# Optimization experiments

Hardware: AMD Instinct MI355X
Metric: run time of the kernel (lower is better)

Reference implementation:

```python
import jax, jax.numpy as jnp
import numpy as np

NUM_HEADS = 12
HEAD_DIM = 64
HIDDEN = NUM_HEADS * HEAD_DIM
AGENT_NUM = 40
MAX_POS = 2048
SCALE = HEAD_DIM ** -0.5


def _split_heads(x):
    # [b, s, hidden] -> [b, h, s, d]
    b, s, _ = x.shape
    return x.reshape(b, s, NUM_HEADS, HEAD_DIM).transpose(0, 2, 1, 3)


def _agent_pool(q, agent_num):
    # F.interpolate(q[None], size=(agent_num, dim), mode='bilinear', align_corners=False)
    # width (dim) is unchanged so it reduces to 1D linear interp along seq axis.
    b, s, dim = q.shape
    src = (jnp.arange(agent_num, dtype=q.dtype) + 0.5) * (s / agent_num) - 0.5
    src = jnp.clip(src, 0.0, s - 1.0)
    lo = jnp.floor(src).astype(jnp.int32)
    hi = jnp.minimum(lo + 1, s - 1)
    w = (src - lo.astype(q.dtype))[None, :, None]  # [1, A, 1]
    return q[:, lo, :] * (1.0 - w) + q[:, hi, :] * w  # [b, A, dim]


def setup_inputs() -> dict:
    key = jax.random.key(0)
    ks = jax.random.split(key, 6)
    bs, S = 16, 2048
    return {
        "hidden_states": jax.random.normal(ks[0], (bs, S, HIDDEN), jnp.float32),
        "attention_mask": jnp.zeros((bs, 1, 1, S), jnp.float32),
        "Wq": jax.random.normal(ks[1], (HIDDEN, HIDDEN), jnp.float32) * 0.02,
        "bq": jnp.zeros((HIDDEN,), jnp.float32),
        "Wk": jax.random.normal(ks[2], (HIDDEN, HIDDEN), jnp.float32) * 0.02,
        "bk": jnp.zeros((HIDDEN,), jnp.float32),
        "Wv": jax.random.normal(ks[3], (HIDDEN, HIDDEN), jnp.float32) * 0.02,
        "bv": jnp.zeros((HIDDEN,), jnp.float32),
        "dist_emb": jax.random.normal(ks[4], (2 * MAX_POS - 1, HEAD_DIM), jnp.float32) * 0.02,
    }


def reference(hidden_states, attention_mask, Wq, bq, Wk, bk, Wv, bv, dist_emb):
    bs, S, dim = hidden_states.shape
    q = hidden_states @ Wq + bq          # [b, S, hidden] (== query_layer flattened back)
    k = hidden_states @ Wk + bk
    v = hidden_states @ Wv + bv
    q_layer = _split_heads(q)            # [b, h, S, d]
    k_layer = _split_heads(k)
    v_layer = _split_heads(v)

    agent = _agent_pool(q, AGENT_NUM)    # [b, A, hidden]
    agent_layer = _split_heads(agent)    # [b, h, A, d]

    # stage 1: agent -> KV, with relative-key position bias
    d1 = jnp.arange(AGENT_NUM)[:, None] - jnp.arange(S)[None, :] + (MAX_POS - 1)
    pe1 = dist_emb[d1]                   # [A, S, d]
    bias1 = jnp.einsum('bhad,asd->bhas', agent_layer, pe1)
    score1 = jnp.einsum('bhad,bhsd->bhas', agent_layer * SCALE, k_layer) + bias1
    score1 = score1 + attention_mask     # [b,1,1,S] broadcasts over (h, A)
    p1 = jax.nn.softmax(score1, axis=-1)
    agent_v = jnp.einsum('bhas,bhsd->bhad', p1, v_layer)  # [b, h, A, d]

    # stage 2: query -> agents, with relative-key position bias
    d2 = jnp.arange(S)[:, None] - jnp.arange(AGENT_NUM)[None, :] + (MAX_POS - 1)
    pe2 = dist_emb[d2]                   # [S, A, d]
    bias2 = jnp.einsum('bhsd,sad->bhsa', q_layer, pe2)
    score2 = jnp.einsum('bhsd,bhad->bhsa', q_layer * SCALE, agent_layer) + bias2
    q_mask = jnp.swapaxes(attention_mask, -1, -2)  # [b,1,S,1]
    score2 = score2 + q_mask
    p2 = jax.nn.softmax(score2, axis=-1)
    x = jnp.einsum('bhsa,bhad->bhsd', p2, agent_v)  # [b, h, S, d]
    return x.transpose(0, 2, 1, 3).reshape(bs, S, dim)
```

## Files before the change

### kernel.cpp

```cpp
#include <hip/hip_runtime.h>
#include <math.h>

#define B_ 16
#define S_ 2048
#define H_ 12
#define D_ 64
#define HID 768
#define A_ 40
#define SCALE_ 0.125f
#define CH1 8
#define SUBT 64
#define NSUB 4

typedef __attribute__((ext_vector_type(8))) short short8v;
typedef __attribute__((ext_vector_type(4))) float f32x4;
typedef __attribute__((ext_vector_type(16))) float f32x16;

__device__ __forceinline__ unsigned f2bf_bits(float x) {
    unsigned u = __float_as_uint(x);
    return (u + 0x7FFFu + ((u >> 16) & 1u)) >> 16;
}

__device__ __forceinline__ void split1(float v, unsigned short& h, unsigned short& l) {
    __bf16 bh = (__bf16)v;
    float hf = (float)bh;
    __bf16 bl = (__bf16)(v - hf);
    h = __builtin_bit_cast(unsigned short, bh);
    l = __builtin_bit_cast(unsigned short, bl);
}

__device__ __forceinline__ void split8c(const float* x, int4& hi, int4& lo) {
    unsigned h[8], l[8];
#pragma unroll
    for (int i = 0; i < 8; i++) {
        __bf16 bh = (__bf16)x[i];
        float hf = (float)bh;
        __bf16 bl = (__bf16)(x[i] - hf);
        h[i] = (unsigned)__builtin_bit_cast(unsigned short, bh);
        l[i] = (unsigned)__builtin_bit_cast(unsigned short, bl);
    }
    hi = make_int4((int)(h[0] | (h[1] << 16)), (int)(h[2] | (h[3] << 16)),
                   (int)(h[4] | (h[5] << 16)), (int)(h[6] | (h[7] << 16)));
    lo = make_int4((int)(l[0] | (l[1] << 16)), (int)(l[2] | (l[3] << 16)),
                   (int)(l[4] | (l[5] << 16)), (int)(l[6] | (l[7] << 16)));
}

__global__ void wt_convert(const float* __restrict__ Wq, const float* __restrict__ Wk,
                           const float* __restrict__ Wv,
                           unsigned short* __restrict__ Wth, unsigned short* __restrict__ Wtl)
{
    int idx = blockIdx.x * 256 + threadIdx.x;
    if (idx >= 3 * 192 * 768) return;
    int n  = idx % 768;
    int kc = (idx / 768) % 192;
    int z  = idx / (768 * 192);
    const float* W = (z == 0) ? Wq : (z == 1) ? Wk : Wv;
    unsigned short h4[4], l4[4];
#pragma unroll
    for (int i = 0; i < 4; i++) {
        float x = W[(size_t)(4 * kc + i) * HID + n];
        unsigned hb = f2bf_bits(x);
        float hf = __uint_as_float(hb << 16);
        h4[i] = (unsigned short)hb;
        l4[i] = (unsigned short)f2bf_bits(x - hf);
    }
    size_t o = ((size_t)z * HID + n) * HID + 4 * kc;
    *(ushort4*)&Wth[o] = make_ushort4(h4[0], h4[1], h4[2], h4[3]);
    *(ushort4*)&Wtl[o] = make_ushort4(l4[0], l4[1], l4[2], l4[3]);
}

__global__ void dist_frag(const float* __restrict__ dist,
                          unsigned short* __restrict__ DFh, unsigned short* __restrict__ DFl)
{
    int g = blockIdx.x * 256 + threadIdx.x;
    if (g >= 256 * 2 * 64) return;
    int lane = g & 63;
    int ks = (g >> 6) & 1;
    int u  = g >> 7;
    int row = 8 + u * 16 + (lane & 15);
    int col = ks * 32 + ((lane >> 4) << 3);
    float xv[8];
#pragma unroll
    for (int j = 0; j < 8; j++)
        xv[j] = (row < 4095) ? dist[(size_t)row * D_ + col + j] : 0.f;
    int4 hi, lo;
    split8c(xv, hi, lo);
    *(int4*)&DFh[(size_t)g * 8] = hi;
    *(int4*)&DFl[(size_t)g * 8] = lo;
}

__global__ void dist_frag0(const float* __restrict__ dist,
                           unsigned short* __restrict__ Dh, unsigned short* __restrict__ Dl)
{
    int g = blockIdx.x * 256 + threadIdx.x;
    if (g >= 131 * 2 * 64) return;
    int lane = g & 63;
    int ks = (g >> 6) & 1;
    int u  = g >> 7;
    int row = u * 16 + (lane & 15);
    int col = ks * 32 + ((lane >> 4) << 3);
    float xv[8];
#pragma unroll
    for (int j = 0; j < 8; j++) xv[j] = dist[(size_t)row * D_ + col + j];
    int4 hi, lo;
    split8c(xv, hi, lo);
    *(int4*)&Dh[(size_t)g * 8] = hi;
    *(int4*)&Dl[(size_t)g * 8] = lo;
}

__global__ void ag_frag(const float* __restrict__ Ag,
                        unsigned short* __restrict__ Gh, unsigned short* __restrict__ Gl,
                        float scale)
{
    int g = blockIdx.x * 256 + threadIdx.x;
    if (g >= 192 * 3 * 2 * 64) return;
    int lane = g & 63;
    int r = g >> 6;
    int ks = r & 1; r >>= 1;
    int at = r % 3;
    int bh = r / 3;
    int a = at * 16 + (lane & 15);
    int col = ks * 32 + ((lane >> 4) << 3);
    float xv[8];
#pragma unroll
    for (int j = 0; j < 8; j++)
        xv[j] = (a < A_) ? scale * Ag[((size_t)bh * A_ + a) * D_ + col + j] : 0.f;
    int4 hi, lo;
    split8c(xv, hi, lo);
    *(int4*)&Gh[(size_t)g * 8] = hi;
    *(int4*)&Gl[(size_t)g * 8] = lo;
}

__global__ void avt_frag(const float* __restrict__ AgV,
                         unsigned short* __restrict__ Vh, unsigned short* __restrict__ Vl)
{
    int g = blockIdx.x * 256 + threadIdx.x;
    if (g >= 192 * 4 * 2 * 64) return;
    int lane = g & 63;
    int r = g >> 6;
    int ks = r & 1; r >>= 1;
    int nt = r & 3;
    int bh = r >> 2;
    int d = nt * 16 + (lane & 15);
    int a0 = ks * 32 + ((lane >> 4) << 3);
    float xv[8];
#pragma unroll
    for (int j = 0; j < 8; j++) {
        int a = a0 + j;
        xv[j] = (a < A_) ? AgV[((size_t)bh * A_ + a) * D_ + d] : 0.f;
    }
    int4 hi, lo;
    split8c(xv, hi, lo);
    *(int4*)&Vh[(size_t)g * 8] = hi;
    *(int4*)&Vl[(size_t)g * 8] = lo;
}

__global__ __launch_bounds__(512, 2) void qkv_z(
    const float* __restrict__ X,
    const unsigned short* __restrict__ Wth, const unsigned short* __restrict__ Wtl,
    const float* __restrict__ bq, const float* __restrict__ bk, const float* __restrict__ bv,
    float* __restrict__ Q, float* __restrict__ K, float* __restrict__ V)
{
    const int L   = blockIdx.x;
    const int k8  = L & 7, sl_ = L >> 3;
    const int mt  = k8 * 32 + sl_ / 9;
    const int sub = sl_ % 9;
    const int nt  = sub % 3, zz = sub / 3;
    const int m0 = mt * 128, n0 = nt * 256;

    const float* __restrict__ bias = (zz == 0) ? bq : (zz == 1) ? bk : bv;
    float* __restrict__ Out        = (zz == 0) ? Q  : (zz == 1) ? K  : V;
    const unsigned short* __restrict__ Bhg = Wth + (size_t)zz * HID * HID;
    const unsigned short* __restrict__ Blg = Wtl + (size_t)zz * HID * HID;

    __shared__ unsigned short Ah[128][40];
    __shared__ unsigned short Al[128][40];
    __shared__ unsigned short Bh[256][40];
    __shared__ unsigned short Bl[256][40];

    const int t = threadIdx.x;
    const int lane = t & 63, w = t >> 6;
    const int wm = (w & 1) * 64, wn = (w >> 1) * 64;
    const int r32 = lane & 31, kh = lane >> 5;

    const int sr = t >> 2, sca = (t & 3) * 8;
    const int sb = t >> 1, scb = (t & 1) * 16;

    f32x16 acc[2][2];
#pragma unroll
    for (int i = 0; i < 2; i++)
#pragma unroll
        for (int j = 0; j < 2; j++)
#pragma unroll
            for (int p = 0; p < 16; p++) acc[i][j][p] = 0.f;

    for (int k0 = 0; k0 < HID; k0 += 32) {
        float xv[8];
        const float* xp = X + (size_t)(m0 + sr) * HID + k0 + sca;
        float4 f0 = *(const float4*)xp;
        float4 f1 = *(const float4*)(xp + 4);
        xv[0] = f0.x; xv[1] = f0.y; xv[2] = f0.z; xv[3] = f0.w;
        xv[4] = f1.x; xv[5] = f1.y; xv[6] = f1.z; xv[7] = f1.w;
        int4 ah, al;
        split8c(xv, ah, al);
        size_t bo = (size_t)(n0 + sb) * HID + k0 + scb;
        int4 bh0 = *(const int4*)&Bhg[bo];
        int4 bh1 = *(const int4*)&Bhg[bo + 8];
        int4 bl0 = *(const int4*)&Blg[bo];
        int4 bl1 = *(const int4*)&Blg[bo + 8];

        __syncthreads();
        *(int4*)&Ah[sr][sca] = ah;
        *(int4*)&Al[sr][sca] = al;
        *(int4*)&Bh[sb][scb]     = bh0;  *(int4*)&Bh[sb][scb + 8] = bh1;
        *(int4*)&Bl[sb][scb]     = bl0;  *(int4*)&Bl[sb][scb + 8] = bl1;
        __syncthreads();

#pragma unroll
        for (int ks = 0; ks < 2; ks++) {
            const int ko = ks * 16 + kh * 8;
            short8v a_h[2], a_l[2], b_h[2], b_l[2];
#pragma unroll
            for (int i = 0; i < 2; i++) {
                a_h[i] = *(const short8v*)&Ah[wm + i * 32 + r32][ko];
                a_l[i] = *(const short8v*)&Al[wm + i * 32 + r32][ko];
                b_h[i] = *(const short8v*)&Bh[wn + i * 32 + r32][ko];
                b_l[i] = *(const short8v*)&Bl[wn + i * 32 + r32][ko];
            }
#pragma unroll
            for (int i = 0; i < 2; i++)
#pragma unroll
                for (int j = 0; j < 2; j++) {
                    acc[i][j] = __builtin_amdgcn_mfma_f32_32x32x16_bf16(a_h[i], b_h[j], acc[i][j], 0, 0, 0);
                    acc[i][j] = __builtin_amdgcn_mfma_f32_32x32x16_bf16(a_l[i], b_h[j], acc[i][j], 0, 0, 0);
                    acc[i][j] = __builtin_amdgcn_mfma_f32_32x32x16_bf16(a_h[i], b_l[j], acc[i][j], 0, 0, 0);
                }
        }
    }

    const float scl = (zz == 1) ? SCALE_ : 1.0f;
#pragma unroll
    for (int j = 0; j < 2; j++) {
        int n = n0 + wn + j * 32 + r32;
        float bj = bias[n];
        int h = n >> 6, d = n & 63;
#pragma unroll
        for (int i = 0; i < 2; i++) {
#pragma unroll
            for (int p = 0; p < 16; p++) {
                int m = m0 + wm + i * 32 + (p & 3) + 8 * (p >> 2) + 4 * kh;
                int b = m >> 11, s = m & 2047;
                Out[(((size_t)b * H_ + h) * S_ + s) * D_ + d] = (acc[i][j][p] + bj) * scl;
            }
        }
    }
}

__global__ void agent_pool(const float* __restrict__ Q, float* __restrict__ Ag)
{
    int idx = blockIdx.x * 256 + threadIdx.x;
    if (idx >= B_ * H_ * A_ * D_) return;
    int d  = idx & 63;
    int a  = (idx >> 6) % A_;
    int bh = idx / (A_ * D_);
    float src = ((float)a + 0.5f) * (2048.0f / 40.0f) - 0.5f;
    src = fminf(fmaxf(src, 0.0f), 2047.0f);
    int lo = (int)floorf(src);
    int hi = min(lo + 1, S_ - 1);
    float w = src - (float)lo;
    const float* base = Q + (size_t)bh * (S_ * D_);
    Ag[idx] = base[lo * D_ + d] * (1.0f - w) + base[hi * D_ + d] * w;
}

__global__ __launch_bounds__(256, 2) void stage1_mfma(
    const float* __restrict__ Kl, const float* __restrict__ Vl,
    const unsigned short* __restrict__ AG1h, const unsigned short* __restrict__ AG1l,
    const unsigned short* __restrict__ D0h,  const unsigned short* __restrict__ D0l,
    const float* __restrict__ mask,
    float* __restrict__ Pacc, float* __restrict__ Pm, float* __restrict__ Pl)
{
    const int q  = blockIdx.x;
    const int bh = blockIdx.y;
    const int b  = bh / H_;
    const int s0 = q * (NSUB * SUBT);
    const float* __restrict__ kb = Kl + (size_t)bh * (S_ * D_);
    const float* __restrict__ vb = Vl + (size_t)bh * (S_ * D_);

    __shared__ unsigned short KFh[4096], KFl[4096];
    __shared__ unsigned short VTh[4096], VTl[4096];
    __shared__ float sc[SUBT][52];
    __shared__ float scp[112][52];
    __shared__ float pm6[6][A_];
    __shared__ float mrow[A_], lrow[A_], resc[A_], mrw[SUBT];

    const int t = threadIdx.x;
    const int lane = t & 63, w = t >> 6;
    const int fr = lane & 15, kg = lane >> 4;

    if (t < A_) { mrow[t] = -INFINITY; lrow[t] = 0.0f; }

    f32x4 acc3[3];
#pragma unroll
    for (int at = 0; at < 3; at++) acc3[at] = (f32x4){0.f, 0.f, 0.f, 0.f};

    for (int st = 0; st < NSUB; st++) {
        const int sb = s0 + st * SUBT;
        const int u0 = (1984 - sb) >> 4;

        __syncthreads();

        {
            const int r = t >> 2, c0 = (t & 3) * 16;
            const float* kp = kb + (size_t)(sb + r) * D_ + c0;
            float xa[8], xb[8];
            float4 f0 = *(const float4*)(kp);
            float4 f1 = *(const float4*)(kp + 4);
            float4 f2 = *(const float4*)(kp + 8);
            float4 f3 = *(const float4*)(kp + 12);
            xa[0]=f0.x; xa[1]=f0.y; xa[2]=f0.z; xa[3]=f0.w;
            xa[4]=f1.x; xa[5]=f1.y; xa[6]=f1.z; xa[7]=f1.w;
            xb[0]=f2.x; xb[1]=f2.y; xb[2]=f2.z; xb[3]=f2.w;
            xb[4]=f3.x; xb[5]=f3.y; xb[6]=f3.z; xb[7]=f3.w;
            int4 h0, l0, h1, l1;
            split8c(xa, h0, l0);
            split8c(xb, h1, l1);
            const int tsr = r >> 4, frr = r & 15;
            const int c8a = (t & 3) * 2, c8b = c8a + 1;
            const int oa = ((tsr * 2 + (c8a >> 2)) * 64 + (((c8a & 3) << 4) | frr)) * 8;
            const int ob = ((tsr * 2 + (c8b >> 2)) * 64 + (((c8b & 3) << 4) | frr)) * 8;
            *(int4*)&KFh[oa] = h0;  *(int4*)&KFl[oa] = l0;
            *(int4*)&KFh[ob] = h1;  *(int4*)&KFl[ob] = l1;
        }
        {
            const int r = t >> 2, c0 = (t & 3) * 16;
            const float* vp = vb + (size_t)(sb + r) * D_ + c0;
            float vv[16];
            float4 g0 = *(const float4*)(vp);
            float4 g1 = *(const float4*)(vp + 4);
            float4 g2 = *(const float4*)(vp + 8);
            float4 g3 = *(const float4*)(vp + 12);
            vv[0]=g0.x; vv[1]=g0.y; vv[2]=g0.z; vv[3]=g0.w;
            vv[4]=g1.x; vv[5]=g1.y; vv[6]=g1.z; vv[7]=g1.w;
            vv[8]=g2.x; vv[9]=g2.y; vv[10]=g2.z; vv[11]=g2.w;
            vv[12]=g3.x; vv[13]=g3.y; vv[14]=g3.z; vv[15]=g3.w;
            const int ks2 = r >> 5, kgp = (r & 31) >> 3, e = r & 7;
#pragma unroll
            for (int jj = 0; jj < 16; jj++) {
                int d = c0 + jj;
                int off = (((d >> 4) * 2 + ks2) * 64 + kgp * 16 + (d & 15)) * 8 + e;
                unsigned short h, l;
                split1(vv[jj], h, l);
                VTh[off] = h; VTl[off] = l;
            }
        }
        if (t < SUBT) mrw[t] = mask[(size_t)b * S_ + sb + t];
        __syncthreads();

        {
            const int ts = w;
#pragma unroll
            for (int at = 0; at < 3; at++) {
                f32x4 a4 = (f32x4){0.f, 0.f, 0.f, 0.f};
#pragma unroll
                for (int ks = 0; ks < 2; ks++) {
                    size_t oA = ((((size_t)bh * 3 + at) * 2 + ks) * 64 + lane) * 8;
                    short8v gh = *(const short8v*)&AG1h[oA];
                    short8v gl = *(const short8v*)&AG1l[oA];
                    short8v kh2 = *(const short8v*)&KFh[((ts * 2 + ks) * 64 + lane) * 8];
                    short8v kl2 = *(const short8v*)&KFl[((ts * 2 + ks) * 64 + lane) * 8];
                    a4 = __builtin_amdgcn_mfma_f32_16x16x32_bf16(gh, kh2, a4, 0, 0, 0);
                    a4 = __builtin_amdgcn_mfma_f32_16x16x32_bf16(gl, kh2, a4, 0, 0, 0);
                    a4 = __builtin_amdgcn_mfma_f32_16x16x32_bf16(gh, kl2, a4, 0, 0, 0);
                }
                *(f32x4*)&sc[ts * 16 + fr][at * 16 + kg * 4] = a4;
            }
        }
        for (int ut = w; ut < 7; ut += 4) {
            const int u = u0 + ut;
#pragma unroll
            for (int at = 0; at < 3; at++) {
                f32x4 a4 = (f32x4){0.f, 0.f, 0.f, 0.f};
#pragma unroll
                for (int ks = 0; ks < 2; ks++) {
                    size_t oA = ((((size_t)bh * 3 + at) * 2 + ks) * 64 + lane) * 8;
                    short8v gh = *(const short8v*)&AG1h[oA];
                    short8v gl = *(const short8v*)&AG1l[oA];
                    size_t oD = (((size_t)u * 2 + ks) * 64 + lane) * 8;
                    short8v dh = *(const short8v*)&D0h[oD];
                    short8v dl = *(const short8v*)&D0l[oD];
                    a4 = __builtin_amdgcn_mfma_f32_16x16x32_bf16(gh, dh, a4, 0, 0, 0);
                    a4 = __builtin_amdgcn_mfma_f32_16x16x32_bf16(gl, dh, a4, 0, 0, 0);
                    a4 = __builtin_amdgcn_mfma_f32_16x16x32_bf16(gh, dl, a4, 0, 0, 0);
                }
                *(f32x4*)&scp[ut * 16 + fr][at * 16 + kg * 4] = a4;
            }
        }
        __syncthreads();

        for (int i = t; i < SUBT * A_; i += 256) {
            int rr = i / 40, aa = i - rr * 40;
            sc[rr][aa] += scp[aa + 63 - rr][aa] + mrw[rr];
        }
        __syncthreads();
        if (t < 240) {
            int a = t % 40, r6 = t / 40;
            float mx = -INFINITY;
            for (int i = r6; i < SUBT; i += 6) mx = fmaxf(mx, sc[i][a]);
            pm6[r6][a] = mx;
        }
        __syncthreads();
        if (t < A_) {
            float lm = pm6[0][t];
#pragma unroll
            for (int r6 = 1; r6 < 6; r6++) lm = fmaxf(lm, pm6[r6][t]);
            float mnew = fmaxf(mrow[t], lm);
            resc[t] = __expf(mrow[t] - mnew);
            mrow[t] = mnew;
        }
        __syncthreads();
        for (int i = t; i < SUBT * A_; i += 256) {
            int rr = i / 40, aa = i - rr * 40;
            sc[rr][aa] = __expf(sc[rr][aa] - mrow[aa]);
        }
        __syncthreads();
        if (t < 240) {
            int a = t % 40, r6 = t / 40;
            float sm = 0.0f;
            for (int i = r6; i < SUBT; i += 6) sm += sc[i][a];
            pm6[r6][a] = sm;
        }
        __syncthreads();
        if (t < A_) {
            float ls = pm6[0][t] + pm6[1][t] + pm6[2][t] + pm6[3][t] + pm6[4][t] + pm6[5][t];
            lrow[t] = lrow[t] * resc[t] + ls;
        }
        __syncthreads();

        for (int g = t; g < 384; g += 256) {
            int pl = g & 63;
            int c = g >> 6;
            int at = c >> 1, ks2 = c & 1;
            int a = at * 16 + (pl & 15);
            int sl0 = ks2 * 32 + (pl >> 4) * 8;
            float xv[8];
#pragma unroll
            for (int e = 0; e < 8; e++)
                xv[e] = (a < A_) ? sc[sl0 + e][a] : 0.f;
            int4 hi, lo;
            split8c(xv, hi, lo);
            *(int4*)&KFh[g * 8] = hi;
            *(int4*)&KFl[g * 8] = lo;
        }
        __syncthreads();

        {
            const int dt = w;
#pragma unroll
            for (int at = 0; at < 3; at++) {
                f32x4 a4 = acc3[at];
#pragma unroll
                for (int p = 0; p < 4; p++) {
                    int a = at * 16 + kg * 4 + p;
                    float rs = (a < A_) ? resc[a] : 0.f;
                    a4[p] *= rs;
                }
#pragma unroll
                for (int ks2 = 0; ks2 < 2; ks2++) {
                    short8v ph = *(const short8v*)&KFh[((at * 2 + ks2) * 64 + lane) * 8];
                    short8v pll = *(const short8v*)&KFl[((at * 2 + ks2) * 64 + lane) * 8];
                    short8v vh = *(const short8v*)&VTh[((dt * 2 + ks2) * 64 + lane) * 8];
                    short8v vl = *(const short8v*)&VTl[((dt * 2 + ks2) * 64 + lane) * 8];
                    a4 = __builtin_amdgcn_mfma_f32_16x16x32_bf16(ph, vh, a4, 0, 0, 0);
                    a4 = __builtin_amdgcn_mfma_f32_16x16x32_bf16(pll, vh, a4, 0, 0, 0);
                    a4 = __builtin_amdgcn_mfma_f32_16x16x32_bf16(ph, vl, a4, 0, 0, 0);
                }
                acc3[at] = a4;
            }
        }
    }
    __syncthreads();

    {
        const int dt = w;
#pragma unroll
        for (int at = 0; at < 3; at++) {
#pragma unroll
            for (int p = 0; p < 4; p++) {
                int a = at * 16 + kg * 4 + p;
                if (a < A_)
                    Pacc[(((size_t)(bh * CH1 + q) * A_) + a) * D_ + dt * 16 + fr] = acc3[at][p];
            }
        }
    }
    if (t < A_) {
        Pm[(size_t)(bh * CH1 + q) * A_ + t] = mrow[t];
        Pl[(size_t)(bh * CH1 + q) * A_ + t] = lrow[t];
    }
}

__global__ __launch_bounds__(256) void stage1_reduce(
    const float* __restrict__ Pacc, const float* __restrict__ Pm,
    const float* __restrict__ Pl, float* __restrict__ AgV)
{
    const int bh = blockIdx.x;
    const int t = threadIdx.x;
    __shared__ float F[CH1][A_], Linv[A_];
    if (t < A_) {
        float M = -INFINITY;
#pragma unroll
        for (int q = 0; q < CH1; q++) M = fmaxf(M, Pm[(size_t)(bh * CH1 + q) * A_ + t]);
        float L = 0.0f;
#pragma unroll
        for (int q = 0; q < CH1; q++) {
            float f = __expf(Pm[(size_t)(bh * CH1 + q) * A_ + t] - M);
            F[q][t] = f;
            L = fmaf(f, Pl[(size_t)(bh * CH1 + q) * A_ + t], L);
        }
        Linv[t] = 1.0f / L;
    }
    __syncthreads();
#pragma unroll
    for (int ii = 0; ii < 3; ii++) {
        int i = t + ii * 256;
        if (i < A_ * 16) {
            int a = i >> 4, d4 = i & 15;
            float4 s4 = make_float4(0.f, 0.f, 0.f, 0.f);
            for (int q = 0; q < CH1; q++) {
                float f = F[q][a];
                float4 p4 = *(const float4*)&Pacc[(((size_t)(bh * CH1 + q) * A_) + a) * D_ + d4 * 4];
                s4.x = fmaf(f, p4.x, s4.x);
                s4.y = fmaf(f, p4.y, s4.y);
                s4.z = fmaf(f, p4.z, s4.z);
                s4.w = fmaf(f, p4.w, s4.w);
            }
            float inv = Linv[a];
            s4.x *= inv; s4.y *= inv; s4.z *= inv; s4.w *= inv;
            *(float4*)&AgV[(size_t)bh * (A_ * D_) + a * D_ + d4 * 4] = s4;
        }
    }
}

__global__ __launch_bounds__(256, 2) void stage2_mfma(
    const float* __restrict__ Qg,
    const unsigned short* __restrict__ AGFh, const unsigned short* __restrict__ AGFl,
    const unsigned short* __restrict__ DFh,  const unsigned short* __restrict__ DFl,
    const unsigned short* __restrict__ AVFh, const unsigned short* __restrict__ AVFl,
    float* __restrict__ Out)
{
    const int sb8 = blockIdx.x;
    const int bh  = blockIdx.y;
    const int b = bh / H_, h = bh % H_;

    __shared__ unsigned short Qfh[8 * 64 * 8], Qfl[8 * 64 * 8];
    __shared__ float scm[64][52];
    __shared__ float scp[64][68];
    __shared__ unsigned short PAh[64][72], PAl[64][72];

    const int t = threadIdx.x;
    const int lane = t & 63, ts = t >> 6;
    const int fr = lane & 15, kg = lane >> 4;

    short8v agh[3][2], agl[3][2];
#pragma unroll
    for (int at = 0; at < 3; at++)
#pragma unroll
        for (int ks = 0; ks < 2; ks++) {
            size_t o = ((((size_t)bh * 3 + at) * 2 + ks) * 64 + lane) * 8;
            agh[at][ks] = *(const short8v*)&AGFh[o];
            agl[at][ks] = *(const short8v*)&AGFl[o];
        }

    const int r = t >> 2, c0 = (t & 3) * 16;
    const int tsr = r >> 4, frr = r & 15;
    const int c8a = (t & 3) * 2, c8b = c8a + 1;
    const int oa = ((tsr * 2 + (c8a >> 2)) * 64 + (((c8a & 3) << 4) | frr)) * 8;
    const int ob = ((tsr * 2 + (c8b >> 2)) * 64 + (((c8b & 3) << 4) | frr)) * 8;
    const float* qbase = Qg + ((size_t)bh * S_ + sb8 * 256 + r) * D_ + c0;

    {
        float4 f0 = *(const float4*)(qbase);
        float4 f1 = *(const float4*)(qbase + 4);
        float4 f2 = *(const float4*)(qbase + 8);
        float4 f3 = *(const float4*)(qbase + 12);
        float xa[8] = {f0.x, f0.y, f0.z, f0.w, f1.x, f1.y, f1.z, f1.w};
        float xb[8] = {f2.x, f2.y, f2.z, f2.w, f3.x, f3.y, f3.z, f3.w};
        int4 h0, l0, h1, l1;
        split8c(xa, h0, l0);
        split8c(xb, h1, l1);
        *(int4*)&Qfh[oa] = h0;  *(int4*)&Qfl[oa] = l0;
        *(int4*)&Qfh[ob] = h1;  *(int4*)&Qfl[ob] = l1;
    }
    __syncthreads();

    for (int c = 0; c < 4; c++) {
        const int s0 = sb8 * 256 + c * 64;
        const int base_u = (s0 >> 4) + 125;

        short8v qh[2], ql[2];
#pragma unroll
        for (int ks = 0; ks < 2; ks++) {
            qh[ks] = *(const short8v*)&Qfh[((ts * 2 + ks) * 64 + lane) * 8];
            ql[ks] = *(const short8v*)&Qfl[((ts * 2 + ks) * 64 + lane) * 8];
        }
        float4 nf0, nf1, nf2, nf3;
        if (c < 3) {
            const float* np = qbase + (size_t)(c + 1) * 64 * D_;
            nf0 = *(const float4*)(np);
            nf1 = *(const float4*)(np + 4);
            nf2 = *(const float4*)(np + 8);
            nf3 = *(const float4*)(np + 12);
        }

#pragma unroll
        for (int at = 0; at < 3; at++) {
            f32x4 acc = (f32x4){0.f, 0.f, 0.f, 0.f};
#pragma unroll
            for (int ks = 0; ks < 2; ks++) {
                acc = __builtin_amdgcn_mfma_f32_16x16x32_bf16(agh[at][ks], qh[ks], acc, 0, 0, 0);
                acc = __builtin_amdgcn_mfma_f32_16x16x32_bf16(agl[at][ks], qh[ks], acc, 0, 0, 0);
                acc = __builtin_amdgcn_mfma_f32_16x16x32_bf16(agh[at][ks], ql[ks], acc, 0, 0, 0);
            }
            *(f32x4*)&scm[ts * 16 + fr][at * 16 + kg * 4] = acc;
        }
#pragma unroll
        for (int o4 = 0; o4 < 4; o4++) {
            f32x4 acc = (f32x4){0.f, 0.f, 0.f, 0.f};
            const int u = base_u + ts + o4;
#pragma unroll
            for (int ks = 0; ks < 2; ks++) {
                size_t o = (((size_t)u * 2 + ks) * 64 + lane) * 8;
                short8v chv = *(const short8v*)&DFh[o];
                short8v clv = *(const short8v*)&DFl[o];
                acc = __builtin_amdgcn_mfma_f32_16x16x32_bf16(chv, qh[ks], acc, 0, 0, 0);
                acc = __builtin_amdgcn_mfma_f32_16x16x32_bf16(clv, qh[ks], acc, 0, 0, 0);
                acc = __builtin_amdgcn_mfma_f32_16x16x32_bf16(chv, ql[ks], acc, 0, 0, 0);
            }
            *(f32x4*)&scp[ts * 16 + fr][o4 * 16 + kg * 4] = acc;
        }
        __syncthreads();

        if (c < 3) {
            float xa[8] = {nf0.x, nf0.y, nf0.z, nf0.w, nf1.x, nf1.y, nf1.z, nf1.w};
            float xb[8] = {nf2.x, nf2.y, nf2.z, nf2.w, nf3.x, nf3.y, nf3.z, nf3.w};
            int4 h0, l0, h1, l1;
            split8c(xa, h0, l0);
            split8c(xb, h1, l1);
            *(int4*)&Qfh[oa] = h0;  *(int4*)&Qfl[oa] = l0;
            *(int4*)&Qfh[ob] = h1;  *(int4*)&Qfl[ob] = l1;
        }
        {
            const int rr = t >> 2, dq = t & 3;
            const int base = (rr & 15) + 39;
            float val[10];
#pragma unroll
            for (int i = 0; i < 10; i++) {
                int a = dq * 10 + i;
                val[i] = scm[rr][a] + scp[rr][base - a];
            }
            float mx = -INFINITY;
#pragma unroll
            for (int i = 0; i < 10; i++) mx = fmaxf(mx, val[i]);
            mx = fmaxf(mx, __shfl_xor(mx, 1));
            mx = fmaxf(mx, __shfl_xor(mx, 2));
            float sum = 0.f;
#pragma unroll
            for (int i = 0; i < 10; i++) { val[i] = __expf(val[i] - mx); sum += val[i]; }
            sum += __shfl_xor(sum, 1);
            sum += __shfl_xor(sum, 2);
            float inv = 1.0f / sum;
            unsigned* ph = (unsigned*)&PAh[rr][0];
            unsigned* pl = (unsigned*)&PAl[rr][0];
#pragma unroll
            for (int i = 0; i < 5; i++) {
                unsigned short h0, l0, h1, l1;
                split1(val[2 * i] * inv, h0, l0);
                split1(val[2 * i + 1] * inv, h1, l1);
                ph[dq * 5 + i] = (unsigned)h0 | ((unsigned)h1 << 16);
                pl[dq * 5 + i] = (unsigned)l0 | ((unsigned)l1 << 16);
            }
#pragma unroll
            for (int i = 0; i < 3; i++) { ph[20 + dq * 3 + i] = 0u; pl[20 + dq * 3 + i] = 0u; }
        }
        __syncthreads();

        short8v ph8[2], pl8[2];
#pragma unroll
        for (int ks = 0; ks < 2; ks++) {
            ph8[ks] = *(const short8v*)&PAh[ts * 16 + fr][ks * 32 + kg * 8];
            pl8[ks] = *(const short8v*)&PAl[ts * 16 + fr][ks * 32 + kg * 8];
        }
#pragma unroll
        for (int nt = 0; nt < 4; nt++) {
            f32x4 acc = (f32x4){0.f, 0.f, 0.f, 0.f};
#pragma unroll
            for (int ks = 0; ks < 2; ks++) {
                size_t o = ((((size_t)bh * 4 + nt) * 2 + ks) * 64 + lane) * 8;
                short8v vh = *(const short8v*)&AVFh[o];
                short8v vl = *(const short8v*)&AVFl[o];
                acc = __builtin_amdgcn_mfma_f32_16x16x32_bf16(ph8[ks], vh, acc, 0, 0, 0);
                acc = __builtin_amdgcn_mfma_f32_16x16x32_bf16(pl8[ks], vh, acc, 0, 0, 0);
                acc = __builtin_amdgcn_mfma_f32_16x16x32_bf16(ph8[ks], vl, acc, 0, 0, 0);
            }
            const int d = nt * 16 + fr;
            float* op = Out + ((size_t)b * S_ + s0 + ts * 16 + kg * 4) * HID + h * D_ + d;
#pragma unroll
            for (int rr = 0; rr < 4; rr++)
                op[(size_t)rr * HID] = acc[rr];
        }
        __syncthreads();
    }
}

extern "C" void kernel_launch(void* const* d_in, const int* in_sizes, int n_in,
                              void* d_out, int out_size, void* d_ws, size_t ws_size,
                              hipStream_t stream) {
    const float* hs   = (const float*)d_in[0];
    const float* mask = (const float*)d_in[1];
    const float* Wq   = (const float*)d_in[2];
    const float* bq   = (const float*)d_in[3];
    const float* Wk   = (const float*)d_in[4];
    const float* bk   = (const float*)d_in[5];
    const float* Wv   = (const float*)d_in[6];
    const float* bv   = (const float*)d_in[7];
    const float* dist = (const float*)d_in[8];
    float* out = (float*)d_out;

    float* ws = (float*)d_ws;
    const size_t QKV = (size_t)B_ * H_ * S_ * D_;
    const size_t AG  = (size_t)B_ * H_ * A_ * D_;
    float* Q     = ws;
    float* K     = ws + QKV;
    float* V     = ws + 2 * QKV;
    float* Agent = ws + 3 * QKV;
    float* AgV   = Agent + AG;
    float* Pacc  = AgV + AG;
    float* Pm    = Pacc + (size_t)B_ * H_ * CH1 * A_ * D_;
    float* Pl    = Pm + (size_t)B_ * H_ * CH1 * A_;
    unsigned short* Wth = (unsigned short*)(Pl + (size_t)B_ * H_ * CH1 * A_);
    unsigned short* Wtl = Wth + (size_t)3 * HID * HID;
    unsigned short* DFh = Wtl + (size_t)3 * HID * HID;
    unsigned short* DFl = DFh + (size_t)262144;
    unsigned short* AGFh = DFl + (size_t)262144;
    unsigned short* AGFl = AGFh + (size_t)589824;
    unsigned short* AVFh = AGFl + (size_t)589824;
    unsigned short* AVFl = AVFh + (size_t)786432;
    unsigned short* AG1h = AVFl + (size_t)786432;
    unsigned short* AG1l = AG1h + (size_t)589824;
    unsigned short* D0h  = AG1l + (size_t)589824;
    unsigned short* D0l  = D0h + (size_t)134144;

    wt_convert<<<(3 * 192 * 768 + 255) / 256, 256, 0, stream>>>(Wq, Wk, Wv, Wth, Wtl);
    dist_frag<<<(256 * 2 * 64 + 255) / 256, 256, 0, stream>>>(dist, DFh, DFl);
    dist_frag0<<<(131 * 2 * 64 + 255) / 256, 256, 0, stream>>>(dist, D0h, D0l);
    qkv_z<<<2304, 512, 0, stream>>>(hs, Wth, Wtl, bq, bk, bv, Q, K, V);
    agent_pool<<<(B_ * H_ * A_ * D_ + 255) / 256, 256, 0, stream>>>(Q, Agent);
    ag_frag<<<(192 * 3 * 2 * 64 + 255) / 256, 256, 0, stream>>>(Agent, AGFh, AGFl, SCALE_);
    ag_frag<<<(192 * 3 * 2 * 64 + 255) / 256, 256, 0, stream>>>(Agent, AG1h, AG1l, 1.0f);
    dim3 g1(CH1, B_ * H_);
    stage1_mfma<<<g1, 256, 0, stream>>>(K, V, AG1h, AG1l, D0h, D0l, mask, Pacc, Pm, Pl);
    stage1_reduce<<<B_ * H_, 256, 0, stream>>>(Pacc, Pm, Pl, AgV);
    avt_frag<<<(192 * 4 * 2 * 64 + 255) / 256, 256, 0, stream>>>(AgV, AVFh, AVFl);
    dim3 g2(8, B_ * H_);
    stage2_mfma<<<g2, 256, 0, stream>>>(Q, AGFh, AGFl, DFh, DFl, AVFh, AVFl, out);
}
```

Before: 563.4 us.

## Merge preconversion kernels, fuse agent pool with fragments, register-load Q in stage2

Three weight and dist conversion kernels are merged into one launch, and agent pooling is fused with both agent fragment conversions in a per-(b,h) kernel using shared memory. Stage2 now loads Q directly into MFMA fragment registers per lane instead of staging through LDS, drops a trailing barrier, and raises the launch-bounds occupancy hint to 3. This cuts launch overhead, intermediate global traffic and LDS/sync cost, at the risk of register pressure from the higher occupancy target and a possible race on the reused shared buffers now that the end-of-loop barrier is gone.

Measured after the change: 582.8 us. 3.4% more time.

```diff
diff --git a/kernel.cpp b/kernel.cpp
--- a/kernel.cpp
+++ b/kernel.cpp
@@ -45,90 +45,68 @@
                    (int)(l[4] | (l[5] << 16)), (int)(l[6] | (l[7] << 16)));
 }
 
-__global__ void wt_convert(const float* __restrict__ Wq, const float* __restrict__ Wk,
-                           const float* __restrict__ Wv,
-                           unsigned short* __restrict__ Wth, unsigned short* __restrict__ Wtl)
+#define WT_BLKS 1728
+#define DF_BLKS 128
+#define D0_BLKS 66
+__global__ __launch_bounds__(256) void preconvert(
+    const float* __restrict__ Wq, const float* __restrict__ Wk, const float* __restrict__ Wv,
+    const float* __restrict__ dist,
+    unsigned short* __restrict__ Wth, unsigned short* __restrict__ Wtl,
+    unsigned short* __restrict__ DFh, unsigned short* __restrict__ DFl,
+    unsigned short* __restrict__ D0h, unsigned short* __restrict__ D0l)
 {
-    int idx = blockIdx.x * 256 + threadIdx.x;
-    if (idx >= 3 * 192 * 768) return;
-    int n  = idx % 768;
-    int kc = (idx / 768) % 192;
-    int z  = idx / (768 * 192);
-    const float* W = (z == 0) ? Wq : (z == 1) ? Wk : Wv;
-    unsigned short h4[4], l4[4];
-#pragma unroll
-    for (int i = 0; i < 4; i++) {
-        float x = W[(size_t)(4 * kc + i) * HID + n];
-        unsigned hb = f2bf_bits(x);
-        float hf = __uint_as_float(hb << 16);
-        h4[i] = (unsigned short)hb;
-        l4[i] = (unsigned short)f2bf_bits(x - hf);
-    }
-    size_t o = ((size_t)z * HID + n) * HID + 4 * kc;
-    *(ushort4*)&Wth[o] = make_ushort4(h4[0], h4[1], h4[2], h4[3]);
-    *(ushort4*)&Wtl[o] = make_ushort4(l4[0], l4[1], l4[2], l4[3]);
-}
-
-__global__ void dist_frag(const float* __restrict__ dist,
-                          unsigned short* __restrict__ DFh, unsigned short* __restrict__ DFl)
-{
-    int g = blockIdx.x * 256 + threadIdx.x;
-    if (g >= 256 * 2 * 64) return;
-    int lane = g & 63;
-    int ks = (g >> 6) & 1;
-    int u  = g >> 7;
-    int row = 8 + u * 16 + (lane & 15);
-    int col = ks * 32 + ((lane >> 4) << 3);
-    float xv[8];
-#pragma unroll
-    for (int j = 0; j < 8; j++)
-        xv[j] = (row < 4095) ? dist[(size_t)row * D_ + col + j] : 0.f;
-    int4 hi, lo;
-    split8c(xv, hi, lo);
-    *(int4*)&DFh[(size_t)g * 8] = hi;
-    *(int4*)&DFl[(size_t)g * 8] = lo;
-}
-
-__global__ void dist_frag0(const float* __restrict__ dist,
-                           unsigned short* __restrict__ Dh, unsigned short* __restrict__ Dl)
-{
-    int g = blockIdx.x * 256 + threadIdx.x;
-    if (g >= 131 * 2 * 64) return;
-    int lane = g & 63;
-    int ks = (g >> 6) & 1;
-    int u  = g >> 7;
-    int row = u * 16 + (lane & 15);
-    int col = ks * 32 + ((lane >> 4) << 3);
-    float xv[8];
-#pragma unroll
-    for (int j = 0; j < 8; j++) xv[j] = dist[(size_t)row * D_ + col + j];
-    int4 hi, lo;
-    split8c(xv, hi, lo);
-    *(int4*)&Dh[(size_t)g * 8] = hi;
-    *(int4*)&Dl[(size_t)g * 8] = lo;
-}
-
-__global__ void ag_frag(const float* __restrict__ Ag,
-                        unsigned short* __restrict__ Gh, unsigned short* __restrict__ Gl,
-                        float scale)
-{
-    int g = blockIdx.x * 256 + threadIdx.x;
-    if (g >= 192 * 3 * 2 * 64) return;
-    int lane = g & 63;
-    int r = g >> 6;
-    int ks = r & 1; r >>= 1;
-    int at = r % 3;
-    int bh = r / 3;
-    int a = at * 16 + (lane & 15);
-    int col = ks * 32 + ((lane >> 4) << 3);
-    float xv[8];
-#pragma unroll
-    for (int j = 0; j < 8; j++)
-        xv[j] = (a < A_) ? scale * Ag[((size_t)bh * A_ + a) * D_ + col + j] : 0.f;
-    int4 hi, lo;
-    split8c(xv, hi, lo);
-    *(int4*)&Gh[(size_t)g * 8] = hi;
-    *(int4*)&Gl[(size_t)g * 8] = lo;
+    const int bx = blockIdx.x;
+    const int t = threadIdx.x;
+    if (bx < WT_BLKS) {
+        int idx = bx * 256 + t;
+        if (idx >= 3 * 192 * 768) return;
+        int n  = idx % 768;
+        int kc = (idx / 768) % 192;
+        int z  = idx / (768 * 192);
+        const float* W = (z == 0) ? Wq : (z == 1) ? Wk : Wv;
+        unsigned short h4[4], l4[4];
+#pragma unroll
+        for (int i = 0; i < 4; i++) {
+            float x = W[(size_t)(4 * kc + i) * HID + n];
+            unsigned hb = f2bf_bits(x);
+            float hf = __uint_as_float(hb << 16);
+            h4[i] = (unsigned short)hb;
+            l4[i] = (unsigned short)f2bf_bits(x - hf);
+        }
+        size_t o = ((size_t)z * HID + n) * HID + 4 * kc;
+        *(ushort4*)&Wth[o] = make_ushort4(h4[0], h4[1], h4[2], h4[3]);
+        *(ushort4*)&Wtl[o] = make_ushort4(l4[0], l4[1], l4[2], l4[3]);
+    } else if (bx < WT_BLKS + DF_BLKS) {
+        int g = (bx - WT_BLKS) * 256 + t;
+        int lane = g & 63;
+        int ks = (g >> 6) & 1;
+        int u  = g >> 7;
+        int row = 8 + u * 16 + (lane & 15);
+        int col = ks * 32 + ((lane >> 4) << 3);
+        float xv[8];
+#pragma unroll
+        for (int j = 0; j < 8; j++)
+            xv[j] = (row < 4095) ? dist[(size_t)row * D_ + col + j] : 0.f;
+        int4 hi, lo;
+        split8c(xv, hi, lo);
+        *(int4*)&DFh[(size_t)g * 8] = hi;
+        *(int4*)&DFl[(size_t)g * 8] = lo;
+    } else {
+        int g = (bx - WT_BLKS - DF_BLKS) * 256 + t;
+        if (g >= 131 * 2 * 64) return;
+        int lane = g & 63;
+        int ks = (g >> 6) & 1;
+        int u  = g >> 7;
+        int row = u * 16 + (lane & 15);
+        int col = ks * 32 + ((lane >> 4) << 3);
+        float xv[8];
+#pragma unroll
+        for (int j = 0; j < 8; j++) xv[j] = dist[(size_t)row * D_ + col + j];
+        int4 hi, lo;
+        split8c(xv, hi, lo);
+        *(int4*)&D0h[(size_t)g * 8] = hi;
+        *(int4*)&D0l[(size_t)g * 8] = lo;
+    }
 }
 
 __global__ void avt_frag(const float* __restrict__ AgV,
@@ -256,20 +234,44 @@
     }
 }
 
-__global__ void agent_pool(const float* __restrict__ Q, float* __restrict__ Ag)
+__global__ __launch_bounds__(256) void agpool_frag(
+    const float* __restrict__ Q,
+    unsigned short* __restrict__ AGFh, unsigned short* __restrict__ AGFl,
+    unsigned short* __restrict__ AG1h, unsigned short* __restrict__ AG1l)
 {
-    int idx = blockIdx.x * 256 + threadIdx.x;
-    if (idx >= B_ * H_ * A_ * D_) return;
-    int d  = idx & 63;
-    int a  = (idx >> 6) % A_;
-    int bh = idx / (A_ * D_);
-    float src = ((float)a + 0.5f) * (2048.0f / 40.0f) - 0.5f;
-    src = fminf(fmaxf(src, 0.0f), 2047.0f);
-    int lo = (int)floorf(src);
-    int hi = min(lo + 1, S_ - 1);
-    float w = src - (float)lo;
+    const int bh = blockIdx.x;
+    const int t = threadIdx.x;
+    __shared__ float ag[A_][D_];
     const float* base = Q + (size_t)bh * (S_ * D_);
-    Ag[idx] = base[lo * D_ + d] * (1.0f - w) + base[hi * D_ + d] * w;
+    for (int i = t; i < A_ * D_; i += 256) {
+        int d = i & 63, a = i >> 6;
+        float src = ((float)a + 0.5f) * (2048.0f / 40.0f) - 0.5f;
+        src = fminf(fmaxf(src, 0.0f), 2047.0f);
+        int lo = (int)floorf(src);
+        int hi = min(lo + 1, S_ - 1);
+        float w = src - (float)lo;
+        ag[a][d] = base[lo * D_ + d] * (1.0f - w) + base[hi * D_ + d] * w;
+    }
+    __syncthreads();
+    for (int g = t; g < 384; g += 256) {
+        int lane = g & 63;
+        int ks = (g >> 6) & 1;
+        int at = g >> 7;
+        int a = at * 16 + (lane & 15);
+        int col = ks * 32 + ((lane >> 4) << 3);
+        float xs[8], x1[8];
+#pragma unroll
+        for (int j = 0; j < 8; j++) {
+            float v = (a < A_) ? ag[a][col + j] : 0.f;
+            x1[j] = v; xs[j] = v * SCALE_;
+        }
+        int4 h1, l1, h2, l2;
+        split8c(xs, h1, l1);
+        split8c(x1, h2, l2);
+        size_t o = ((((size_t)bh * 3 + at) * 2 + ks) * 64 + lane) * 8;
+        *(int4*)&AGFh[o] = h1;  *(int4*)&AGFl[o] = l1;
+        *(int4*)&AG1h[o] = h2;  *(int4*)&AG1l[o] = l2;
+    }
 }
 
 __global__ __launch_bounds__(256, 2) void stage1_mfma(
@@ -540,7 +542,7 @@
     }
 }
 
-__global__ __launch_bounds__(256, 2) void stage2_mfma(
+__global__ __launch_bounds__(256, 3) void stage2_mfma(
     const float* __restrict__ Qg,
     const unsigned short* __restrict__ AGFh, const unsigned short* __restrict__ AGFl,
     const unsigned short* __restrict__ DFh,  const unsigned short* __restrict__ DFl,
@@ -551,7 +553,6 @@
     const int bh  = blockIdx.y;
     const int b = bh / H_, h = bh % H_;
 
-    __shared__ unsigned short Qfh[8 * 64 * 8], Qfl[8 * 64 * 8];
     __shared__ float scm[64][52];
     __shared__ float scp[64][68];
     __shared__ unsigned short PAh[64][72], PAl[64][72];
@@ -570,45 +571,32 @@
             agl[at][ks] = *(const short8v*)&AGFl[o];
         }
 
-    const int r = t >> 2, c0 = (t & 3) * 16;
-    const int tsr = r >> 4, frr = r & 15;
-    const int c8a = (t & 3) * 2, c8b = c8a + 1;
-    const int oa = ((tsr * 2 + (c8a >> 2)) * 64 + (((c8a & 3) << 4) | frr)) * 8;
-    const int ob = ((tsr * 2 + (c8b >> 2)) * 64 + (((c8b & 3) << 4) | frr)) * 8;
-    const float* qbase = Qg + ((size_t)bh * S_ + sb8 * 256 + r) * D_ + c0;
-
-    {
-        float4 f0 = *(const float4*)(qbase);
-        float4 f1 = *(const float4*)(qbase + 4);
-        float4 f2 = *(const float4*)(qbase + 8);
-        float4 f3 = *(const float4*)(qbase + 12);
+    const float* qlane = Qg + ((size_t)bh * S_ + sb8 * 256 + ts * 16 + fr) * D_ + kg * 8;
+
+    float4 f0 = *(const float4*)(qlane);
+    float4 f1 = *(const float4*)(qlane + 4);
+    float4 f2 = *(const float4*)(qlane + 32);
+    float4 f3 = *(const float4*)(qlane + 36);
+
+    for (int c = 0; c < 4; c++) {
+        const int s0 = sb8 * 256 + c * 64;
+        const int base_u = (s0 >> 4) + 125;
+
         float xa[8] = {f0.x, f0.y, f0.z, f0.w, f1.x, f1.y, f1.z, f1.w};
         float xb[8] = {f2.x, f2.y, f2.z, f2.w, f3.x, f3.y, f3.z, f3.w};
         int4 h0, l0, h1, l1;
         split8c(xa, h0, l0);
         split8c(xb, h1, l1);
-        *(int4*)&Qfh[oa] = h0;  *(int4*)&Qfl[oa] = l0;
-        *(int4*)&Qfh[ob] = h1;  *(int4*)&Qfl[ob] = l1;
-    }
-    __syncthreads();
-
-    for (int c = 0; c < 4; c++) {
-        const int s0 = sb8 * 256 + c * 64;
-        const int base_u = (s0 >> 4) + 125;
-
         short8v qh[2], ql[2];
-#pragma unroll
-        for (int ks = 0; ks < 2; ks++) {
-            qh[ks] = *(const short8v*)&Qfh[((ts * 2 + ks) * 64 + lane) * 8];
-            ql[ks] = *(const short8v*)&Qfl[((ts * 2 + ks) * 64 + lane) * 8];
-        }
-        float4 nf0, nf1, nf2, nf3;
+        qh[0] = __builtin_bit_cast(short8v, h0);  ql[0] = __builtin_bit_cast(short8v, l0);
+        qh[1] = __builtin_bit_cast(short8v, h1);  ql[1] = __builtin_bit_cast(short8v, l1);
+
         if (c < 3) {
-            const float* np = qbase + (size_t)(c + 1) * 64 * D_;
-            nf0 = *(const float4*)(np);
-            nf1 = *(const float4*)(np + 4);
-            nf2 = *(const float4*)(np + 8);
-            nf3 = *(const float4*)(np + 12);
+            const float* np = qlane + (size_t)(c + 1) * 64 * D_;
+            f0 = *(const float4*)(np);
+            f1 = *(const float4*)(np + 4);
+            f2 = *(const float4*)(np + 32);
+            f3 = *(const float4*)(np + 36);
         }
 
 #pragma unroll
@@ -639,15 +627,6 @@
         }
         __syncthreads();
 
-        if (c < 3) {
-            float xa[8] = {nf0.x, nf0.y, nf0.z, nf0.w, nf1.x, nf1.y, nf1.z, nf1.w};
-            float xb[8] = {nf2.x, nf2.y, nf2.z, nf2.w, nf3.x, nf3.y, nf3.z, nf3.w};
-            int4 h0, l0, h1, l1;
-            split8c(xa, h0, l0);
-            split8c(xb, h1, l1);
-            *(int4*)&Qfh[oa] = h0;  *(int4*)&Qfl[oa] = l0;
-            *(int4*)&Qfh[ob] = h1;  *(int4*)&Qfl[ob] = l1;
-        }
         {
             const int rr = t >> 2, dq = t & 3;
             const int base = (rr & 15) + 39;
@@ -672,11 +651,11 @@
             unsigned* pl = (unsigned*)&PAl[rr][0];
 #pragma unroll
             for (int i = 0; i < 5; i++) {
-                unsigned short h0, l0, h1, l1;
-                split1(val[2 * i] * inv, h0, l0);
-                split1(val[2 * i + 1] * inv, h1, l1);
-                ph[dq * 5 + i] = (unsigned)h0 | ((unsigned)h1 << 16);
-                pl[dq * 5 + i] = (unsigned)l0 | ((unsigned)l1 << 16);
+                unsigned short hh0, ll0, hh1, ll1;
+                split1(val[2 * i] * inv, hh0, ll0);
+                split1(val[2 * i + 1] * inv, hh1, ll1);
+                ph[dq * 5 + i] = (unsigned)hh0 | ((unsigned)hh1 << 16);
+                pl[dq * 5 + i] = (unsigned)ll0 | ((unsigned)ll1 << 16);
             }
 #pragma unroll
             for (int i = 0; i < 3; i++) { ph[20 + dq * 3 + i] = 0u; pl[20 + dq * 3 + i] = 0u; }
@@ -707,7 +686,6 @@
             for (int rr = 0; rr < 4; rr++)
                 op[(size_t)rr * HID] = acc[rr];
         }
-        __syncthreads();
     }
 }
 
@@ -749,13 +727,10 @@
     unsigned short* D0h  = AG1l + (size_t)589824;
     unsigned short* D0l  = D0h + (size_t)134144;
 
-    wt_convert<<<(3 * 192 * 768 + 255) / 256, 256, 0, stream>>>(Wq, Wk, Wv, Wth, Wtl);
-    dist_frag<<<(256 * 2 * 64 + 255) / 256, 256, 0, stream>>>(dist, DFh, DFl);
-    dist_frag0<<<(131 * 2 * 64 + 255) / 256, 256, 0, stream>>>(dist, D0h, D0l);
+    preconvert<<<WT_BLKS + DF_BLKS + D0_BLKS, 256, 0, stream>>>(
+        Wq, Wk, Wv, dist, Wth, Wtl, DFh, DFl, D0h, D0l);
     qkv_z<<<2304, 512, 0, stream>>>(hs, Wth, Wtl, bq, bk, bv, Q, K, V);
-    agent_pool<<<(B_ * H_ * A_ * D_ + 255) / 256, 256, 0, stream>>>(Q, Agent);
-    ag_frag<<<(192 * 3 * 2 * 64 + 255) / 256, 256, 0, stream>>>(Agent, AGFh, AGFl, SCALE_);
-    ag_frag<<<(192 * 3 * 2 * 64 + 255) / 256, 256, 0, stream>>>(Agent, AG1h, AG1l, 1.0f);
+    agpool_frag<<<B_ * H_, 256, 0, stream>>>(Q, AGFh, AGFl, AG1h, AG1l);
     dim3 g1(CH1, B_ * H_);
     stage1_mfma<<<g1, 256, 0, stream>>>(K, V, AG1h, AG1l, D0h, D0l, mask, Pacc, Pm, Pl);
     stage1_reduce<<<B_ * H_, 256, 0, stream>>>(Pacc, Pm, Pl, AgV);
```
